# Performance work log

Measured on AMD Instinct MI355X. Metric: run time of the kernel, lower is better.

## Reference

```python
import jax, jax.numpy as jnp
import numpy as np


def setup_inputs() -> dict:
    key = jax.random.key(0)
    ks = jax.random.split(key, 6)
    Bsz, Ch, N, L = 16, 1024, 16, 4096
    return {
        "input": jax.random.normal(ks[0], (Bsz, Ch, L), jnp.float32),
        "A": jax.random.normal(ks[1], (Ch, N, 2), jnp.float32),
        "B": jax.random.normal(ks[2], (Ch, N), jnp.float32),  # unused in 'dws' mode
        "C": jax.random.normal(ks[3], (Ch, N), jnp.float32),  # unused in 'dws' mode
        "log_dt": jax.random.normal(ks[4], (Ch, N), jnp.float32) * 0.5 - 4.0,
        "E": jax.random.normal(ks[5], (Ch, N), jnp.float32),
    }


def reference(input, A, B, C, log_dt, E):
    """Kernelizer forward, mode='dws', run_mode='training'.

    discretize (simplified ZOH):
      A_real = -softplus(A[...,0]); A_imag = A[...,1]; dt = exp(log_dt)
      E_hat = E * dt; dtA = dt * (A_real + i*A_imag)        # (Ch, N)
    kernel: k[c, l] = Re( sum_n E_hat[c,n] * exp(dtA[c,n] * l) )
    output: causal depthwise conv of input with k via 2L-padded FFT.
    """
    L = input.shape[-1]
    A_real = -jax.nn.softplus(A[..., 0])                     # (Ch, N)
    A_imag = A[..., 1]                                       # (Ch, N)
    dt = jnp.exp(log_dt)                                     # (Ch, N)
    E_hat = E * dt                                           # (Ch, N)
    dtA_real = dt * A_real
    dtA_imag = dt * A_imag

    l = jnp.arange(L, dtype=input.dtype)                     # (L,)
    # real part of the complex vandermonde, fused: exp(ar*l) * cos(ai*l)
    vand = jnp.exp(dtA_real[:, :, None] * l) * jnp.cos(dtA_imag[:, :, None] * l)  # (Ch, N, L)
    k = jnp.einsum('cn,cnl->cl', E_hat, vand)                # (Ch, L)

    n_fft = 2 * L  # zero-pad so circular conv == linear causal conv
    Uf = jnp.fft.rfft(input, n=n_fft)                        # (B, Ch, L+1)
    Kf = jnp.fft.rfft(k, n=n_fft)                            # (Ch, L+1)
    y = jnp.fft.irfft(Uf * Kf, n=n_fft)[..., :L]             # (B, Ch, L)
    return y.astype(input.dtype)
```

## Files before the change

kernel.cpp:

```cpp
#include <hip/hip_runtime.h>
#include <hip/hip_bf16.h>

#define CH   1024
#define LSEQ 4096
#define NST  16

typedef __attribute__((ext_vector_type(8))) short short8;
typedef __attribute__((ext_vector_type(4))) float f32x4;

__device__ __forceinline__ unsigned int pkrn(float a, float b) {
    __hip_bfloat162 h = __float22bfloat162_rn(make_float2(a, b));
    unsigned int u;
    __builtin_memcpy(&u, &h, 4);
    return u;
}
#define DSHR(x, d) __int_as_float(__builtin_amdgcn_update_dpp(0, __float_as_int(x), 0x110 + (d), 0xf, 0xf, true))
__device__ __forceinline__ float swz15(float x) {
    return __int_as_float(__builtin_amdgcn_ds_swizzle(__float_as_int(x), 0x1F0));
}

#define XT0_OFF  0
#define XT1_OFF  8192
#define SIN0_OFF 16384
#define SIN1_OFF 20480
#define TBL_OFF  16384
#define EH_OFF   24704
#define SMEM_SZ  25024

__device__ __forceinline__ void barrier_fast() {
    asm volatile("s_waitcnt lgkmcnt(0)\n\ts_barrier" ::: "memory");
}

__global__ __launch_bounds__(256, 4) void conv_k(const float* __restrict__ x,
                                                 const float* __restrict__ A,
                                                 const float* __restrict__ log_dt,
                                                 const float* __restrict__ E,
                                                 float* __restrict__ y) {
    __shared__ __align__(16) char smem[SMEM_SZ];
    const int tid  = threadIdx.x;
    const int w    = tid >> 6, lane = tid & 63;
    const int g    = lane >> 4, l15 = lane & 15;
    const int a    = w >> 1, s = w & 1;
    const int bid  = blockIdx.x;
    const int c    = bid >> 1;
    const int half = bid & 1;

    const size_t cstride = (size_t)CH * LSEQ;
    const float* xr = x + ((size_t)(8 * half) * CH + c) * (size_t)LSEQ;
    float*       yb = y + ((size_t)(8 * half) * CH + c) * (size_t)LSEQ;

    int stb[2];
#pragma unroll
    for (int it = 0; it < 2; ++it) {
        int slot = it * 256 + tid;
        int m = slot >> 3, js = slot & 7;
        stb[it] = (m * 128 + js * 16) ^ ((m & 7) << 4);
    }
    float4 pend[4];
    auto ldraw = [&](const float* xp) {
#pragma unroll
        for (int it = 0; it < 2; ++it) {
            int slot = it * 256 + tid;
            pend[2 * it]     = *(const float4*)(xp + slot * 8);
            pend[2 * it + 1] = *(const float4*)(xp + slot * 8 + 4);
        }
    };
    auto stage = [&](int xoff) {
#pragma unroll
        for (int it = 0; it < 2; ++it) {
            uint4 pk;
            pk.x = pkrn(pend[2 * it].x,     pend[2 * it].y);
            pk.y = pkrn(pend[2 * it].z,     pend[2 * it].w);
            pk.z = pkrn(pend[2 * it + 1].x, pend[2 * it + 1].y);
            pk.w = pkrn(pend[2 * it + 1].z, pend[2 * it + 1].w);
            *(uint4*)(smem + xoff + stb[it]) = pk;
        }
    };

    ldraw(xr);

    float* PR = (float*)(smem + TBL_OFF);
    float* PI = PR + NST * 65;
    float* EH = (float*)(smem + EH_OFF);
    float* KL = EH + NST;
    {
        int n = tid & 15;
        int idx0 = c * NST + n;
        float a0 = A[2 * idx0], a1 = A[2 * idx0 + 1];
        float sp = (a0 > 20.f) ? a0 : log1pf(expf(a0));
        float dtv = expf(log_dt[idx0]);
        float dar = -dtv * sp, dai = dtv * a1;
        if (tid < NST) EH[tid] = E[idx0] * dtv;
        for (int l = tid >> 4; l < 65; l += 16) {
            float mg = expf(dar * (float)l);
            float sn, cs;
            sincosf(dai * (float)l, &sn, &cs);
            PR[n * 65 + l] = mg * cs;
            PI[n * 65 + l] = mg * sn;
        }
    }
    __syncthreads();
    if (tid < 64) {
        float kl = 0.f;
#pragma unroll
        for (int nn = 0; nn < NST; ++nn) kl += EH[nn] * PR[nn * 65 + tid];
        KL[tid] = kl;
    }
    __syncthreads();

    short8 wa[2], pa[3];
    {
        int p = 16 * a + l15;
        const float* tb = ((p & 1) ? PI : PR) + (p >> 1) * 65;
#pragma unroll
        for (int kt = 0; kt < 2; ++kt) {
            union { short8 v; unsigned int d[4]; } u;
#pragma unroll
            for (int e2 = 0; e2 < 4; ++e2) {
                int j = kt * 32 + 8 * g + 2 * e2;
                u.d[e2] = pkrn(tb[63 - j], tb[62 - j]);
            }
            wa[kt] = u.v;
        }
        int i = 16 * w + l15;
#pragma unroll
        for (int kt = 0; kt < 2; ++kt) {
            union { short8 v; unsigned int d[4]; } u;
#pragma unroll
            for (int e2 = 0; e2 < 4; ++e2) {
                int k0 = kt * 32 + 8 * g + 2 * e2;
                float v0 = (k0 <= i)     ? KL[i - k0]     : 0.f;
                float v1 = (k0 + 1 <= i) ? KL[i - k0 - 1] : 0.f;
                u.d[e2] = pkrn(v0, v1);
            }
            pa[kt] = u.v;
        }
        {
            union { short8 v; unsigned int d[4]; } u;
#pragma unroll
            for (int e2 = 0; e2 < 4; ++e2) {
                int n3 = 4 * g + e2;
                float re = EH[n3] * PR[n3 * 65 + i + 1];
                float im = -EH[n3] * PI[n3 * 65 + i + 1];
                u.d[e2] = pkrn(re, im);
            }
            pa[2] = u.v;
        }
    }

    float q1r, q1i, q2r, q2i, q4r, q4i, q8r, q8i, fr_, fi_;
    {
        int nq = 8 * a + 2 * g + s;
        q1r = PR[nq * 65 + 64];
        q1i = PI[nq * 65 + 64];
        q2r = fmaf(q1r, q1r, -(q1i * q1i)); q2i = 2.f * q1r * q1i;
        q4r = fmaf(q2r, q2r, -(q2i * q2i)); q4i = 2.f * q2r * q2i;
        q8r = fmaf(q4r, q4r, -(q4i * q4i)); q8i = 2.f * q4r * q4i;
        float cr = q1r, ci = q1i;
        { float tr = fmaf(cr, q1r, -(ci * q1i)), ti = fmaf(cr, q1i, ci * q1r);
          cr = (l15 & 1) ? tr : cr; ci = (l15 & 1) ? ti : ci; }
        { float tr = fmaf(cr, q2r, -(ci * q2i)), ti = fmaf(cr, q2i, ci * q2r);
          cr = (l15 & 2) ? tr : cr; ci = (l15 & 2) ? ti : ci; }
        { float tr = fmaf(cr, q4r, -(ci * q4i)), ti = fmaf(cr, q4i, ci * q4r);
          cr = (l15 & 4) ? tr : cr; ci = (l15 & 4) ? ti : ci; }
        { float tr = fmaf(cr, q8r, -(ci * q8i)), ti = fmaf(cr, q8i, ci * q8r);
          cr = (l15 & 8) ? tr : cr; ci = (l15 & 8) ? ti : ci; }
        fr_ = cr; fi_ = ci;
    }

    int xfo[4][2], sino[4];
#pragma unroll
    for (int nt = 0; nt < 4; ++nt) {
#pragma unroll
        for (int kt = 0; kt < 2; ++kt)
            xfo[nt][kt] = ((l15 * 128 + kt * 64 + g * 16) ^ ((l15 & 7) << 4)) + nt * 2048;
        sino[nt] = ((l15 * 64 + g * 16) ^ ((l15 & 3) << 4)) + nt * 1024;
    }
    const int sinwb = (l15 * 64 + 8 * g + 32 * a + 4 * s) ^ ((l15 & 3) << 4);

    stage(XT0_OFF);
    ldraw(xr + cstride);
    __syncthreads();

    f32x4 acc[4];
    const f32x4 z = {0.f, 0.f, 0.f, 0.f};
    int cur = XT0_OFF, nxt = XT1_OFF;

#pragma unroll 1
    for (int bb = 0; bb < 8; ++bb) {
        const int sb = (bb & 1) ? SIN1_OFF : SIN0_OFF;
        if (bb > 0) {
            const int sbp = (bb & 1) ? SIN0_OFF : SIN1_OFF;
            float* yr = yb + (size_t)(bb - 1) * cstride;
#pragma unroll
            for (int nt = 0; nt < 4; ++nt) {
                short8 sf = *(const short8*)(smem + sbp + sino[nt]);
                acc[nt] = __builtin_amdgcn_mfma_f32_16x16x32_bf16(pa[2], sf, acc[nt], 0, 0, 0);
            }
#pragma unroll
            for (int nt = 0; nt < 4; ++nt) {
                int m = l15 + 16 * nt;
                float4 v = make_float4(acc[nt][0], acc[nt][1], acc[nt][2], acc[nt][3]);
                *(float4*)(yr + m * 64 + 16 * w + 4 * g) = v;
            }
        }

        short8 xf[4][2];
#pragma unroll
        for (int nt = 0; nt < 4; ++nt)
#pragma unroll
            for (int kt = 0; kt < 2; ++kt)
                xf[nt][kt] = *(const short8*)(smem + cur + xfo[nt][kt]);

        f32x4 sa[4];
#pragma unroll
        for (int nt = 0; nt < 4; ++nt) {
            sa[nt] = __builtin_amdgcn_mfma_f32_16x16x32_bf16(wa[0], xf[nt][0], z, 0, 0, 0);
            sa[nt] = __builtin_amdgcn_mfma_f32_16x16x32_bf16(wa[1], xf[nt][1], sa[nt], 0, 0, 0);
        }
#pragma unroll
        for (int nt = 0; nt < 4; ++nt)
            acc[nt] = __builtin_amdgcn_mfma_f32_16x16x32_bf16(pa[0], xf[nt][0], z, 0, 0, 0);
        if (w >= 2) {
#pragma unroll
            for (int nt = 0; nt < 4; ++nt)
                acc[nt] = __builtin_amdgcn_mfma_f32_16x16x32_bf16(pa[1], xf[nt][1], acc[nt], 0, 0, 0);
        }

        float pr[4], pi[4];
#pragma unroll
        for (int nt = 0; nt < 4; ++nt) {
            pr[nt] = s ? sa[nt][2] : sa[nt][0];
            pi[nt] = s ? sa[nt][3] : sa[nt][1];
        }
#pragma unroll
        for (int nt = 0; nt < 4; ++nt) {
            { float ur = DSHR(pr[nt], 1), ui = DSHR(pi[nt], 1);
              pr[nt] = fmaf(q1r, ur, fmaf(-q1i, ui, pr[nt]));
              pi[nt] = fmaf(q1r, ui, fmaf(q1i, ur, pi[nt])); }
            { float ur = DSHR(pr[nt], 2), ui = DSHR(pi[nt], 2);
              pr[nt] = fmaf(q2r, ur, fmaf(-q2i, ui, pr[nt]));
              pi[nt] = fmaf(q2r, ui, fmaf(q2i, ur, pi[nt])); }
            { float ur = DSHR(pr[nt], 4), ui = DSHR(pi[nt], 4);
              pr[nt] = fmaf(q4r, ur, fmaf(-q4i, ui, pr[nt]));
              pi[nt] = fmaf(q4r, ui, fmaf(q4i, ur, pi[nt])); }
            { float ur = DSHR(pr[nt], 8), ui = DSHR(pi[nt], 8);
              pr[nt] = fmaf(q8r, ur, fmaf(-q8i, ui, pr[nt]));
              pi[nt] = fmaf(q8r, ui, fmaf(q8i, ur, pi[nt])); }
        }
        float bR[3], bI[3];
#pragma unroll
        for (int nt = 1; nt < 4; ++nt) {
            bR[nt - 1] = swz15(pr[nt - 1]);
            bI[nt - 1] = swz15(pi[nt - 1]);
            pr[nt] = fmaf(fr_, bR[nt - 1], fmaf(-fi_, bI[nt - 1], pr[nt]));
            pi[nt] = fmaf(fr_, bI[nt - 1], fmaf(fi_, bR[nt - 1], pi[nt]));
        }
#pragma unroll
        for (int nt = 0; nt < 4; ++nt) {
            float eR = DSHR(pr[nt], 1), eI = DSHR(pi[nt], 1);
            float b0R = (nt == 0) ? 0.f : bR[nt - 1];
            float b0I = (nt == 0) ? 0.f : bI[nt - 1];
            eR = (l15 == 0) ? b0R : eR;
            eI = (l15 == 0) ? b0I : eI;
            *(unsigned int*)(smem + sb + sinwb + nt * 1024) = pkrn(eR, eI);
        }

        if (bb < 7) stage(nxt);
        if (bb < 6) ldraw(xr + (size_t)(bb + 2) * cstride);

        barrier_fast();
        int t = cur; cur = nxt; nxt = t;
    }

    {
        const int sbp = SIN1_OFF;
        float* yr = yb + (size_t)7 * cstride;
#pragma unroll
        for (int nt = 0; nt < 4; ++nt) {
            short8 sf = *(const short8*)(smem + sbp + sino[nt]);
            acc[nt] = __builtin_amdgcn_mfma_f32_16x16x32_bf16(pa[2], sf, acc[nt], 0, 0, 0);
        }
#pragma unroll
        for (int nt = 0; nt < 4; ++nt) {
            int m = l15 + 16 * nt;
            float4 v = make_float4(acc[nt][0], acc[nt][1], acc[nt][2], acc[nt][3]);
            *(float4*)(yr + m * 64 + 16 * w + 4 * g) = v;
        }
    }
}

extern "C" void kernel_launch(void* const* d_in, const int* in_sizes, int n_in,
                              void* d_out, int out_size, void* d_ws, size_t ws_size,
                              hipStream_t stream) {
    const float* x      = (const float*)d_in[0];
    const float* A      = (const float*)d_in[1];
    const float* log_dt = (const float*)d_in[4];
    const float* E      = (const float*)d_in[5];
    float* out = (float*)d_out;
    (void)d_ws; (void)ws_size;

    conv_k<<<2 * CH, 256, 0, stream>>>(x, A, log_dt, E, out);
}
```

Measured before the change: 110.8 us.

## Shorten cross-tile scan dependency chain and split MFMA accumulation chains

```diff
diff --git a/kernel.cpp b/kernel.cpp
--- a/kernel.cpp
+++ b/kernel.cpp
@@ -148,7 +148,7 @@
         }
     }
 
-    float q1r, q1i, q2r, q2i, q4r, q4i, q8r, q8i, fr_, fi_;
+    float q1r, q1i, q2r, q2i, q4r, q4i, q8r, q8i, q16r, q16i, fr_, fi_;
     {
         int nq = 8 * a + 2 * g + s;
         q1r = PR[nq * 65 + 64];
@@ -156,6 +156,7 @@
         q2r = fmaf(q1r, q1r, -(q1i * q1i)); q2i = 2.f * q1r * q1i;
         q4r = fmaf(q2r, q2r, -(q2i * q2i)); q4i = 2.f * q2r * q2i;
         q8r = fmaf(q4r, q4r, -(q4i * q4i)); q8i = 2.f * q4r * q4i;
+        q16r = fmaf(q8r, q8r, -(q8i * q8i)); q16i = 2.f * q8r * q8i;
         float cr = q1r, ci = q1i;
         { float tr = fmaf(cr, q1r, -(ci * q1i)), ti = fmaf(cr, q1i, ci * q1r);
           cr = (l15 & 1) ? tr : cr; ci = (l15 & 1) ? ti : ci; }
@@ -188,7 +189,13 @@
 
 #pragma unroll 1
     for (int bb = 0; bb < 8; ++bb) {
-        const int sb = (bb & 1) ? SIN1_OFF : SIN0_OFF;
+        short8 xf[4][2];
+#pragma unroll
+        for (int nt = 0; nt < 4; ++nt)
+#pragma unroll
+            for (int kt = 0; kt < 2; ++kt)
+                xf[nt][kt] = *(const short8*)(smem + cur + xfo[nt][kt]);
+
         if (bb > 0) {
             const int sbp = (bb & 1) ? SIN0_OFF : SIN1_OFF;
             float* yr = yb + (size_t)(bb - 1) * cstride;
@@ -205,18 +212,13 @@
             }
         }
 
-        short8 xf[4][2];
-#pragma unroll
-        for (int nt = 0; nt < 4; ++nt)
-#pragma unroll
-            for (int kt = 0; kt < 2; ++kt)
-                xf[nt][kt] = *(const short8*)(smem + cur + xfo[nt][kt]);
-
-        f32x4 sa[4];
-#pragma unroll
-        for (int nt = 0; nt < 4; ++nt) {
-            sa[nt] = __builtin_amdgcn_mfma_f32_16x16x32_bf16(wa[0], xf[nt][0], z, 0, 0, 0);
-            sa[nt] = __builtin_amdgcn_mfma_f32_16x16x32_bf16(wa[1], xf[nt][1], sa[nt], 0, 0, 0);
+        float pr[4], pi[4];
+#pragma unroll
+        for (int nt = 0; nt < 4; ++nt) {
+            f32x4 sa = __builtin_amdgcn_mfma_f32_16x16x32_bf16(wa[0], xf[nt][0], z, 0, 0, 0);
+            f32x4 sc = __builtin_amdgcn_mfma_f32_16x16x32_bf16(wa[1], xf[nt][1], z, 0, 0, 0);
+            pr[nt] = s ? (sa[2] + sc[2]) : (sa[0] + sc[0]);
+            pi[nt] = s ? (sa[3] + sc[3]) : (sa[1] + sc[1]);
         }
 #pragma unroll
         for (int nt = 0; nt < 4; ++nt)
@@ -227,12 +229,6 @@
                 acc[nt] = __builtin_amdgcn_mfma_f32_16x16x32_bf16(pa[1], xf[nt][1], acc[nt], 0, 0, 0);
         }
 
-        float pr[4], pi[4];
-#pragma unroll
-        for (int nt = 0; nt < 4; ++nt) {
-            pr[nt] = s ? sa[nt][2] : sa[nt][0];
-            pi[nt] = s ? sa[nt][3] : sa[nt][1];
-        }
 #pragma unroll
         for (int nt = 0; nt < 4; ++nt) {
             { float ur = DSHR(pr[nt], 1), ui = DSHR(pi[nt], 1);
@@ -248,19 +244,30 @@
               pr[nt] = fmaf(q8r, ur, fmaf(-q8i, ui, pr[nt]));
               pi[nt] = fmaf(q8r, ui, fmaf(q8i, ur, pi[nt])); }
         }
-        float bR[3], bI[3];
+        float tR[3], tI[3];
+#pragma unroll
+        for (int nt = 0; nt < 3; ++nt) {
+            tR[nt] = swz15(pr[nt]);
+            tI[nt] = swz15(pi[nt]);
+        }
+        float TR[3], TI_[3];
+        TR[0] = tR[0]; TI_[0] = tI[0];
+#pragma unroll
+        for (int nt = 1; nt < 3; ++nt) {
+            TR[nt]  = fmaf(q16r, TR[nt - 1], fmaf(-q16i, TI_[nt - 1], tR[nt]));
+            TI_[nt] = fmaf(q16r, TI_[nt - 1], fmaf(q16i, TR[nt - 1], tI[nt]));
+        }
 #pragma unroll
         for (int nt = 1; nt < 4; ++nt) {
-            bR[nt - 1] = swz15(pr[nt - 1]);
-            bI[nt - 1] = swz15(pi[nt - 1]);
-            pr[nt] = fmaf(fr_, bR[nt - 1], fmaf(-fi_, bI[nt - 1], pr[nt]));
-            pi[nt] = fmaf(fr_, bI[nt - 1], fmaf(fi_, bR[nt - 1], pi[nt]));
-        }
+            pr[nt] = fmaf(fr_, TR[nt - 1], fmaf(-fi_, TI_[nt - 1], pr[nt]));
+            pi[nt] = fmaf(fr_, TI_[nt - 1], fmaf(fi_, TR[nt - 1], pi[nt]));
+        }
+        const int sb = (bb & 1) ? SIN1_OFF : SIN0_OFF;
 #pragma unroll
         for (int nt = 0; nt < 4; ++nt) {
             float eR = DSHR(pr[nt], 1), eI = DSHR(pi[nt], 1);
-            float b0R = (nt == 0) ? 0.f : bR[nt - 1];
-            float b0I = (nt == 0) ? 0.f : bI[nt - 1];
+            float b0R = (nt == 0) ? 0.f : TR[nt - 1];
+            float b0I = (nt == 0) ? 0.f : TI_[nt - 1];
             eR = (l15 == 0) ? b0R : eR;
             eI = (l15 == 0) ? b0I : eI;
             *(unsigned int*)(smem + sb + sinwb + nt * 1024) = pkrn(eR, eI);
```

Measured after the change: 139.0 us. 25.5% more time.
